# Kernel optimization log

Hardware: AMD Instinct MI355X
Metric: run time of the kernel (lower is better)

The kernel has to match this reference:

```python
import jax, jax.numpy as jnp
import numpy as np

N_NODES = 100000
N_EDGES = 3200000
N_GRAPHS = 64
F_IN = 16
HID = 64


def gcn_conv(x, W, b, src, dst, ew, n_nodes):
    """PyG GCNConv with add_self_loops=True, symmetric normalization.
    x' = D^{-1/2} (A + I) D^{-1/2} (x W) + b, self-loop weight 1."""
    h = x @ W                                             # [N, out]
    deg = jax.ops.segment_sum(ew, dst, num_segments=n_nodes) + 1.0  # self-loop adds 1
    dinv = jax.lax.rsqrt(jnp.maximum(deg, 1e-12))         # deg_inv_sqrt
    norm = dinv[src] * ew * dinv[dst]                     # [E]
    agg = jax.ops.segment_sum(h[src] * norm[:, None], dst, num_segments=n_nodes)
    agg = agg + h * (dinv * dinv)[:, None]                # self-loop term
    return agg + b


def setup_inputs() -> dict:
    key = jax.random.key(0)
    ks = jax.random.split(key, 12)
    x = jax.random.normal(ks[0], (N_NODES, F_IN), dtype=jnp.float32)
    edge_index = jax.random.randint(ks[1], (2, N_EDGES), 0, N_NODES, dtype=jnp.int64)
    edge_weight = jax.random.uniform(ks[2], (N_EDGES,), dtype=jnp.float32)
    batch = jnp.sort(jax.random.randint(ks[3], (N_NODES,), 0, N_GRAPHS, dtype=jnp.int64))
    # GCN layer params (PyG lin: x @ W with W [in, out])
    s1 = 1.0 / np.sqrt(F_IN)
    s2 = 1.0 / np.sqrt(HID)
    W1 = jax.random.uniform(ks[4], (F_IN, HID), jnp.float32, -s1, s1)
    b1 = jnp.zeros((HID,), jnp.float32)
    W2 = jax.random.uniform(ks[5], (HID, HID), jnp.float32, -s2, s2)
    b2 = jnp.zeros((HID,), jnp.float32)
    W3 = jax.random.uniform(ks[6], (HID, HID), jnp.float32, -s2, s2)
    b3 = jnp.zeros((HID,), jnp.float32)
    Wout = jax.random.uniform(ks[7], (HID, 1), jnp.float32, -s2, s2)
    bout = jax.random.uniform(ks[8], (1,), jnp.float32, -s2, s2)
    return {"x": x, "edge_index": edge_index, "edge_weight": edge_weight,
            "batch": batch, "W1": W1, "b1": b1, "W2": W2, "b2": b2,
            "W3": W3, "b3": b3, "Wout": Wout, "bout": bout}


def reference(x, edge_index, edge_weight, batch, W1, b1, W2, b2, W3, b3, Wout, bout):
    src, dst = edge_index[0], edge_index[1]
    n = x.shape[0]
    # layer 1
    h = gcn_conv(x, W1, b1, src, dst, edge_weight, n)
    # layer 2: sigmoid -> (dropout p=0 identity) -> GCNConv
    h = gcn_conv(jax.nn.sigmoid(h), W2, b2, src, dst, edge_weight, n)
    # layer 3
    h = gcn_conv(jax.nn.sigmoid(h), W3, b3, src, dst, edge_weight, n)
    # global mean pool over graphs
    sums = jax.ops.segment_sum(h, batch, num_segments=N_GRAPHS)          # [G, HID]
    counts = jax.ops.segment_sum(jnp.ones((n,), h.dtype), batch, num_segments=N_GRAPHS)
    pooled = sums / jnp.maximum(counts, 1.0)[:, None]
    # final linear head (dropout p=0 identity)
    return pooled @ Wout + bout                                          # [G, 1]
```

## Files before the change

kernel.cpp:

```cpp
#include <hip/hip_runtime.h>
#include <hip/hip_bf16.h>

#define HID 64
#define P_BLOCKS 1024
#define MAXB 512
#define BCAP 9216
#define TILE 3200
#define AGRID 2048

typedef float v2f __attribute__((ext_vector_type(2)));

__device__ inline v2f fp8x2_lo(unsigned u) { return __builtin_amdgcn_cvt_pk_f32_fp8(u, false); }
__device__ inline v2f fp8x2_hi(unsigned u) { return __builtin_amdgcn_cvt_pk_f32_fp8(u, true); }

#define GSCALE 16.0f
#define GINV 0.0625f
#define GS1 12.0f
#define GI1 (1.0f / 12.0f)
#define GS2 24.0f
#define GI2 (1.0f / 24.0f)
#define WQINV (1.0f / 4095.0f)

__global__ __launch_bounds__(256) void kp1a_hist(const int* __restrict__ dst,
                                                 int* __restrict__ ghist,
                                                 int nE, int B, int chunk) {
    __shared__ int h[MAXB];
    for (int b = threadIdx.x; b < B; b += 256) h[b] = 0;
    __syncthreads();
    int lo = blockIdx.x * chunk;
    int hi = min(nE, lo + chunk);
    for (int i = lo + threadIdx.x; i < hi; i += 256)
        atomicAdd(&h[dst[i] >> 8], 1);
    __syncthreads();
    for (int b = threadIdx.x; b < B; b += 256)
        ghist[(size_t)b * P_BLOCKS + blockIdx.x] = h[b];
}

__global__ __launch_bounds__(256) void kp1b1_scan(const int* __restrict__ ghist,
                                                  int* __restrict__ goff,
                                                  int* __restrict__ btot) {
    __shared__ int wsum[4];
    __shared__ int woff[4];
    int tid = threadIdx.x;
    int lane = tid & 63, wv = tid >> 6;
    int b = blockIdx.x;
    int4 v = ((const int4*)(ghist + (size_t)b * P_BLOCKS))[tid];
    int s = v.x + v.y + v.z + v.w;
    int sc = s;
#pragma unroll
    for (int off = 1; off < 64; off <<= 1) {
        int t = __shfl_up(sc, off);
        if (lane >= off) sc += t;
    }
    if (lane == 63) wsum[wv] = sc;
    __syncthreads();
    if (tid == 0) {
        int acc = 0;
#pragma unroll
        for (int w = 0; w < 4; ++w) { woff[w] = acc; acc += wsum[w]; }
        btot[b] = acc;
    }
    __syncthreads();
    int ex = woff[wv] + sc - s;
    int4 o;
    o.x = ex;
    o.y = ex + v.x;
    o.z = o.y + v.y;
    o.w = o.z + v.z;
    ((int4*)(goff + (size_t)b * P_BLOCKS))[tid] = o;
}

__global__ __launch_bounds__(512) void kp1b2_scan(const int* __restrict__ btot,
                                                  int* __restrict__ bstart, int B) {
    __shared__ int wsum[8];
    __shared__ int woff[8];
    int tid = threadIdx.x;
    int lane = tid & 63, wv = tid >> 6;
    int tot = (tid < B) ? btot[tid] : 0;
    int sc = tot;
#pragma unroll
    for (int off = 1; off < 64; off <<= 1) {
        int t = __shfl_up(sc, off);
        if (lane >= off) sc += t;
    }
    if (lane == 63) wsum[wv] = sc;
    __syncthreads();
    if (tid == 0) {
        int acc = 0;
#pragma unroll
        for (int w = 0; w < 8; ++w) { woff[w] = acc; acc += wsum[w]; }
        bstart[B] = acc;
    }
    __syncthreads();
    if (tid < B) bstart[tid] = woff[wv] + sc - tot;
}

__global__ __launch_bounds__(256) void kp1c_sort(const int* __restrict__ src,
                                                 const int* __restrict__ dst,
                                                 const float* __restrict__ ew,
                                                 const int* __restrict__ goff,
                                                 const int* __restrict__ bstart,
                                                 int2* __restrict__ bsw,
                                                 int nE, int B, int chunk) {
    __shared__ int2 sorted[TILE];
    __shared__ unsigned short bkt[TILE];
    __shared__ int cnt[MAXB];
    __shared__ int lstart[MAXB];
    __shared__ int lcur[MAXB];
    __shared__ int gcur[MAXB];
    __shared__ int wsum[4];
    __shared__ int woff[4];
    int tid = threadIdx.x;
    int lane = tid & 63, wv = tid >> 6;
    for (int b = tid; b < B; b += 256)
        gcur[b] = bstart[b] + goff[(size_t)b * P_BLOCKS + blockIdx.x];
    int lo = blockIdx.x * chunk;
    int hi = min(nE, lo + chunk);
    for (int tb = lo; tb < hi; tb += TILE) {
        int m = min(hi - tb, TILE);
        cnt[tid] = 0;
        cnt[tid + 256] = 0;
        __syncthreads();
        for (int i = tid; i < m; i += 256)
            atomicAdd(&cnt[dst[tb + i] >> 8], 1);
        __syncthreads();
        int c0 = cnt[2 * tid], c1 = cnt[2 * tid + 1];
        int s = c0 + c1;
        int sc = s;
#pragma unroll
        for (int off = 1; off < 64; off <<= 1) {
            int t = __shfl_up(sc, off);
            if (lane >= off) sc += t;
        }
        if (lane == 63) wsum[wv] = sc;
        __syncthreads();
        if (tid == 0) {
            int acc = 0;
#pragma unroll
            for (int w = 0; w < 4; ++w) { woff[w] = acc; acc += wsum[w]; }
        }
        __syncthreads();
        int ex = woff[wv] + sc - s;
        lstart[2 * tid] = ex;
        lcur[2 * tid] = ex;
        lstart[2 * tid + 1] = ex + c0;
        lcur[2 * tid + 1] = ex + c0;
        __syncthreads();
        for (int i = tid; i < m; i += 256) {
            int d = dst[tb + i];
            int b = d >> 8;
            int pos = atomicAdd(&lcur[b], 1);
            int2 v;
            v.x = src[tb + i] | ((d & 255) << 20);
            v.y = __float_as_int(ew[tb + i]);
            sorted[pos] = v;
            bkt[pos] = (unsigned short)b;
        }
        __syncthreads();
        for (int i = tid; i < m; i += 256) {
            int b = bkt[i];
            bsw[gcur[b] + (i - lstart[b])] = sorted[i];
        }
        __syncthreads();
        for (int b = tid; b < B; b += 256)
            gcur[b] += lcur[b] - lstart[b];
        __syncthreads();
    }
}

__global__ __launch_bounds__(256) void kp2_build(const int2* __restrict__ bsw,
                                                 const int* __restrict__ bstart,
                                                 int* __restrict__ row_start,
                                                 float* __restrict__ dinv,
                                                 unsigned* __restrict__ csr4,
                                                 int n_nodes) {
    __shared__ int2 ebuf[BCAP];
    __shared__ int cnt[256];
    __shared__ float degw[256];
    __shared__ int cur[256];
    __shared__ int wsum[4];
    __shared__ int woff[4];
    int tid = threadIdx.x;
    int lane = tid & 63, wv = tid >> 6;
    int b = blockIdx.x;
    int e0 = bstart[b], e1 = bstart[b + 1];
    int nb = e1 - e0;
    cnt[tid] = 0;
    degw[tid] = 0.0f;
    __syncthreads();
    for (int i = tid; i < nb; i += 256) {
        int2 v = bsw[e0 + i];
        if (i < BCAP) ebuf[i] = v;
        int dlo = (v.x >> 20) & 255;
        atomicAdd(&cnt[dlo], 1);
        atomicAdd(&degw[dlo], __int_as_float(v.y));
    }
    __syncthreads();
    int c = cnt[tid];
    int sc = c;
#pragma unroll
    for (int off = 1; off < 64; off <<= 1) {
        int t = __shfl_up(sc, off);
        if (lane >= off) sc += t;
    }
    if (lane == 63) wsum[wv] = sc;
    __syncthreads();
    if (tid == 0) {
        int acc = 0;
#pragma unroll
        for (int w = 0; w < 4; ++w) { woff[w] = acc; acc += wsum[w]; }
    }
    __syncthreads();
    int ex = woff[wv] + sc - c;
    cur[tid] = ex;
    int node = (b << 8) + tid;
    if (node < n_nodes) {
        row_start[node] = e0 + ex;
        dinv[node] = rsqrtf(fmaxf(degw[tid] + 1.0f, 1e-12f));
    }
    if (b == 0 && tid == 0) row_start[n_nodes] = bstart[gridDim.x];
    __syncthreads();
    for (int i = tid; i < nb; i += 256) {
        int2 v = (i < BCAP) ? ebuf[i] : bsw[e0 + i];
        int dlo = (v.x >> 20) & 255;
        int pos = atomicAdd(&cur[dlo], 1);
        float w = __int_as_float(v.y);
        unsigned wq = (unsigned)(w * 4095.0f + 0.5f);
        csr4[e0 + pos] = ((unsigned)v.x & 0xFFFFFu) | (wq << 20);
    }
}

__global__ __launch_bounds__(64) void k_wtilde(const float* __restrict__ W3,
                                               const float* __restrict__ Wout,
                                               const float* __restrict__ b3,
                                               float* __restrict__ wtil,
                                               float* __restrict__ c0) {
    int j = threadIdx.x;
    float s = 0.0f;
    for (int k = 0; k < 64; ++k) s += W3[j * 64 + k] * Wout[k];
    wtil[j] = s;
    if (j == 0) {
        float c = 0.0f;
        for (int k = 0; k < 64; ++k) c += b3[k] * Wout[k];
        c0[0] = c;
    }
}

__global__ __launch_bounds__(256) void k_mm16f4(const float* __restrict__ in,
                                                const float* __restrict__ W,
                                                const float* __restrict__ dinv,
                                                unsigned* __restrict__ gtab,
                                                int n_nodes) {
    __shared__ float Ws[16 * HID];
    for (int i = threadIdx.x; i < 16 * HID; i += 256) Ws[i] = W[i];
    __syncthreads();
    int lane = threadIdx.x & 63;
    int wid = threadIdx.x >> 6;
    int p = lane & 7;
    int q = lane >> 3;
    int nGrp = (n_nodes + 7) >> 3;
    for (int grp = blockIdx.x * 4 + wid; grp < nGrp; grp += gridDim.x * 4) {
        int node = grp * 8 + q;
        bool ok = node < n_nodes;
        float xr0 = ok ? in[node * 16 + p] : 0.0f;
        float xr1 = ok ? in[node * 16 + 8 + p] : 0.0f;
        float di = ok ? dinv[node] : 0.0f;
        v2f a01 = {0.0f, 0.0f}, a23 = {0.0f, 0.0f};
        v2f a45 = {0.0f, 0.0f}, a67 = {0.0f, 0.0f};
#pragma unroll
        for (int k = 0; k < 16; ++k) {
            float xv = __shfl((k < 8) ? xr0 : xr1, q * 8 + (k & 7));
            const float4* wr = (const float4*)&Ws[k * HID + 8 * p];
            float4 w0 = wr[0], w1 = wr[1];
            v2f wl0 = {w0.x, w0.y}, wl1 = {w0.z, w0.w};
            v2f wl2 = {w1.x, w1.y}, wl3 = {w1.z, w1.w};
            a01 += wl0 * xv; a23 += wl1 * xv; a45 += wl2 * xv; a67 += wl3 * xv;
        }
        float sc = di * GS1;
        unsigned pk = __builtin_amdgcn_cvt_scalef32_pk_fp4_f32(0u, a01.x * sc, a01.y * sc, 1.0f, 0);
        pk = __builtin_amdgcn_cvt_scalef32_pk_fp4_f32(pk, a23.x * sc, a23.y * sc, 1.0f, 1);
        pk = __builtin_amdgcn_cvt_scalef32_pk_fp4_f32(pk, a45.x * sc, a45.y * sc, 1.0f, 2);
        pk = __builtin_amdgcn_cvt_scalef32_pk_fp4_f32(pk, a67.x * sc, a67.y * sc, 1.0f, 3);
        if (ok) gtab[(size_t)node * 8 + p] = pk;
    }
}

template <int OUT4>
__global__ __launch_bounds__(256) void k_agg4(const unsigned* __restrict__ g4,
                                              const float* __restrict__ bias,
                                              const float* __restrict__ dinv,
                                              const int* __restrict__ row_start,
                                              const unsigned* __restrict__ csr4,
                                              const float* __restrict__ Wn,
                                              void* __restrict__ outv,
                                              int n_nodes, float ginv_in, float gs_out) {
    int lane = threadIdx.x & 63;
    int wid = threadIdx.x >> 6;
    int p = lane & 7;
    int q = lane >> 3;
    int stride = gridDim.x * 4;

    for (int node = blockIdx.x * 4 + wid; node < n_nodes; node += stride) {
        float diRaw = dinv[node];

        v2f a01 = {0.0f, 0.0f}, a23 = {0.0f, 0.0f};
        v2f a45 = {0.0f, 0.0f}, a67 = {0.0f, 0.0f};
        {
            unsigned su = g4[(size_t)node * 8 + p];
            if (q == 0) {
                a01 = __builtin_amdgcn_cvt_scalef32_pk_f32_fp4(su, 1.0f, 0);
                a23 = __builtin_amdgcn_cvt_scalef32_pk_f32_fp4(su, 1.0f, 1);
                a45 = __builtin_amdgcn_cvt_scalef32_pk_f32_fp4(su, 1.0f, 2);
                a67 = __builtin_amdgcn_cvt_scalef32_pk_f32_fp4(su, 1.0f, 3);
            }
        }
        int e0 = row_start[node], e1 = row_start[node + 1];
        for (int base = e0; base < e1; base += 64) {
            int m = min(64, e1 - base);
            unsigned sw = 0;
            if (lane < m) sw = __builtin_nontemporal_load(csr4 + base + lane);
            int ng8 = (m + 7) >> 3;
            int ng84 = (ng8 + 3) & ~3;
            for (int g0 = 0; g0 < ng84; g0 += 4) {
                int b8 = 8 * g0 + q;
                unsigned vA = __shfl(sw, b8);
                unsigned vB = __shfl(sw, b8 + 8);
                unsigned vC = __shfl(sw, b8 + 16);
                unsigned vD = __shfl(sw, b8 + 24);
                unsigned uA = g4[(vA & 0xFFFFFu) * 8u + p];
                unsigned uB = g4[(vB & 0xFFFFFu) * 8u + p];
                unsigned uC = g4[(vC & 0xFFFFFu) * 8u + p];
                unsigned uD = g4[(vD & 0xFFFFFu) * 8u + p];
                float wA = (float)(vA >> 20) * WQINV;
                float wB = (float)(vB >> 20) * WQINV;
                float wC = (float)(vC >> 20) * WQINV;
                float wD = (float)(vD >> 20) * WQINV;
                a01 += __builtin_amdgcn_cvt_scalef32_pk_f32_fp4(uA, 1.0f, 0) * wA;
                a23 += __builtin_amdgcn_cvt_scalef32_pk_f32_fp4(uA, 1.0f, 1) * wA;
                a45 += __builtin_amdgcn_cvt_scalef32_pk_f32_fp4(uA, 1.0f, 2) * wA;
                a67 += __builtin_amdgcn_cvt_scalef32_pk_f32_fp4(uA, 1.0f, 3) * wA;
                a01 += __builtin_amdgcn_cvt_scalef32_pk_f32_fp4(uB, 1.0f, 0) * wB;
                a23 += __builtin_amdgcn_cvt_scalef32_pk_f32_fp4(uB, 1.0f, 1) * wB;
                a45 += __builtin_amdgcn_cvt_scalef32_pk_f32_fp4(uB, 1.0f, 2) * wB;
                a67 += __builtin_amdgcn_cvt_scalef32_pk_f32_fp4(uB, 1.0f, 3) * wB;
                a01 += __builtin_amdgcn_cvt_scalef32_pk_f32_fp4(uC, 1.0f, 0) * wC;
                a23 += __builtin_amdgcn_cvt_scalef32_pk_f32_fp4(uC, 1.0f, 1) * wC;
                a45 += __builtin_amdgcn_cvt_scalef32_pk_f32_fp4(uC, 1.0f, 2) * wC;
                a67 += __builtin_amdgcn_cvt_scalef32_pk_f32_fp4(uC, 1.0f, 3) * wC;
                a01 += __builtin_amdgcn_cvt_scalef32_pk_f32_fp4(uD, 1.0f, 0) * wD;
                a23 += __builtin_amdgcn_cvt_scalef32_pk_f32_fp4(uD, 1.0f, 1) * wD;
                a45 += __builtin_amdgcn_cvt_scalef32_pk_f32_fp4(uD, 1.0f, 2) * wD;
                a67 += __builtin_amdgcn_cvt_scalef32_pk_f32_fp4(uD, 1.0f, 3) * wD;
            }
        }
        float a[8] = {a01.x, a01.y, a23.x, a23.y, a45.x, a45.y, a67.x, a67.y};
#pragma unroll
        for (int i = 0; i < 8; ++i) {
            a[i] += __shfl_xor(a[i], 8);
            a[i] += __shfl_xor(a[i], 16);
            a[i] += __shfl_xor(a[i], 32);
        }
        float di = diRaw * ginv_in;
        float4 bv0 = ((const float4*)bias)[2 * p];
        float4 bv1 = ((const float4*)bias)[2 * p + 1];
        a[0] = fmaf(di, a[0], bv0.x); a[1] = fmaf(di, a[1], bv0.y);
        a[2] = fmaf(di, a[2], bv0.z); a[3] = fmaf(di, a[3], bv0.w);
        a[4] = fmaf(di, a[4], bv1.x); a[5] = fmaf(di, a[5], bv1.y);
        a[6] = fmaf(di, a[6], bv1.z); a[7] = fmaf(di, a[7], bv1.w);
        float s[8];
#pragma unroll
        for (int i = 0; i < 8; ++i) s[i] = 1.0f / (1.0f + __expf(-a[i]));

        if (OUT4) {
            const float4* Wg = (const float4*)Wn;
            v2f o01 = {0.0f, 0.0f}, o23 = {0.0f, 0.0f};
            v2f o45 = {0.0f, 0.0f}, o67 = {0.0f, 0.0f};
#pragma unroll
            for (int st = 0; st < 8; ++st) {
                float av = __shfl(s[st], q);
                const float4* wr = Wg + ((8 * q + st) * 16 + 2 * p);
                float4 w0 = wr[0], w1 = wr[1];
                v2f wl0 = {w0.x, w0.y}, wl1 = {w0.z, w0.w};
                v2f wl2 = {w1.x, w1.y}, wl3 = {w1.z, w1.w};
                o01 += wl0 * av; o23 += wl1 * av; o45 += wl2 * av; o67 += wl3 * av;
            }
            float o[8] = {o01.x, o01.y, o23.x, o23.y, o45.x, o45.y, o67.x, o67.y};
#pragma unroll
            for (int i = 0; i < 8; ++i) {
                o[i] += __shfl_xor(o[i], 8);
                o[i] += __shfl_xor(o[i], 16);
                o[i] += __shfl_xor(o[i], 32);
            }
            if (lane < 8) {
                float sc = diRaw * gs_out;
                unsigned pk = __builtin_amdgcn_cvt_scalef32_pk_fp4_f32(0u, o[0] * sc, o[1] * sc, 1.0f, 0);
                pk = __builtin_amdgcn_cvt_scalef32_pk_fp4_f32(pk, o[2] * sc, o[3] * sc, 1.0f, 1);
                pk = __builtin_amdgcn_cvt_scalef32_pk_fp4_f32(pk, o[4] * sc, o[5] * sc, 1.0f, 2);
                pk = __builtin_amdgcn_cvt_scalef32_pk_fp4_f32(pk, o[6] * sc, o[7] * sc, 1.0f, 3);
                __builtin_nontemporal_store(pk, (unsigned*)outv + (size_t)node * 8 + p);
            }
        } else {
            const float4* wt4 = (const float4*)Wn;
            float4 w0 = wt4[2 * p], w1 = wt4[2 * p + 1];
            float local = s[0] * w0.x + s[1] * w0.y + s[2] * w0.z + s[3] * w0.w
                        + s[4] * w1.x + s[5] * w1.y + s[6] * w1.z + s[7] * w1.w;
            local += __shfl_xor(local, 1);
            local += __shfl_xor(local, 2);
            local += __shfl_xor(local, 4);
            if (lane == 0) {
                unsigned pk = __builtin_amdgcn_cvt_pk_fp8_f32(local * diRaw * gs_out, 0.0f, 0, false);
                ((unsigned char*)outv)[node] = (unsigned char)(pk & 0xFFu);
            }
        }
    }
}

__global__ __launch_bounds__(256) void k_agg3s(const unsigned char* __restrict__ t8,
                                               const int* __restrict__ row_start,
                                               const float* __restrict__ dinv,
                                               const unsigned* __restrict__ csr4,
                                               const float* __restrict__ c0p,
                                               float* __restrict__ p,
                                               int n_nodes) {
    int lane = threadIdx.x & 63;
    int wid = threadIdx.x >> 6;
    int stride = gridDim.x * 4;
    float c0 = c0p[0];
    for (int node = blockIdx.x * 4 + wid; node < n_nodes; node += stride) {
        int e0 = row_start[node], e1 = row_start[node + 1];
        float acc = 0.0f;
        for (int base = e0; base < e1; base += 64) {
            int i = base + lane;
            unsigned sw = (i < e1) ? __builtin_nontemporal_load(csr4 + i) : 0u;
            float tv = fp8x2_lo((unsigned)t8[sw & 0xFFFFFu]).x;
            acc += (float)(sw >> 20) * tv;
        }
        acc *= WQINV;
#pragma unroll
        for (int off = 32; off; off >>= 1) acc += __shfl_xor(acc, off);
        if (lane == 0) {
            float self = fp8x2_lo((unsigned)t8[node]).x;
            p[node] = fmaf(dinv[node] * GINV, acc + self, c0);
        }
    }
}

__global__ __launch_bounds__(256) void k_poolseg(const float* __restrict__ p,
                                                 const int* __restrict__ batch,
                                                 float* __restrict__ psum,
                                                 float* __restrict__ pcnt,
                                                 int n_nodes) {
    int lane = threadIdx.x & 63;
    int gw = (blockIdx.x * blockDim.x + threadIdx.x) >> 6;
    int node = gw * 64 + lane;
    bool valid = node < n_nodes;
    float v = valid ? p[node] : 0.0f;
    int g = valid ? batch[node] : -1;
    int g0 = __shfl(g, 0);
    if (__all((g == g0) && valid)) {
#pragma unroll
        for (int off = 32; off; off >>= 1) v += __shfl_xor(v, off);
        if (lane == 0) {
            atomicAdd(&psum[g0], v);
            atomicAdd(&pcnt[g0], 64.0f);
        }
    } else if (valid) {
        atomicAdd(&psum[g], v);
        atomicAdd(&pcnt[g], 1.0f);
    }
}

__global__ __launch_bounds__(64) void k_out(const float* __restrict__ psum,
                                            const float* __restrict__ pcnt,
                                            const float* __restrict__ bout,
                                            float* __restrict__ out, int G) {
    int g = threadIdx.x;
    if (g < G) out[g] = psum[g] / fmaxf(pcnt[g], 1.0f) + bout[0];
}

extern "C" void kernel_launch(void* const* d_in, const int* in_sizes, int n_in,
                              void* d_out, int out_size, void* d_ws, size_t ws_size,
                              hipStream_t stream) {
    const float* x    = (const float*)d_in[0];
    const int*   eidx = (const int*)d_in[1];
    const float* ew   = (const float*)d_in[2];
    const int*   batch= (const int*)d_in[3];
    const float* W1   = (const float*)d_in[4];
    const float* b1   = (const float*)d_in[5];
    const float* W2   = (const float*)d_in[6];
    const float* b2   = (const float*)d_in[7];
    const float* W3   = (const float*)d_in[8];
    const float* b3   = (const float*)d_in[9];
    const float* Wout = (const float*)d_in[10];
    const float* bout = (const float*)d_in[11];
    float* out = (float*)d_out;

    const int N = in_sizes[0] / 16;
    const int E = in_sizes[2];
    const int G = out_size;
    const int* src = eidx;
    const int* dst = eidx + E;
    const int B = (N + 255) >> 8;
    const int chunk = (E + P_BLOCKS - 1) / P_BLOCKS;

    size_t off = 0;
    auto carve = [&](size_t bytes) -> void* {
        void* p = (char*)d_ws + off;
        off += (bytes + 255) & ~(size_t)255;
        return p;
    };
    float* psum     = (float*)carve(64 * 4);
    float* pcnt     = (float*)carve(64 * 4);
    size_t zero_bytes = off;
    int*   ghist    = (int*)  carve((size_t)B * P_BLOCKS * 4);
    int*   goff     = (int*)  carve((size_t)B * P_BLOCKS * 4);
    int*   btot    = (int*)  carve((size_t)B * 4);
    int*   bstart   = (int*)  carve((size_t)(B + 1) * 4);
    int2*  bsw      = (int2*) carve((size_t)E * 8);
    int*   row_start= (int*)  carve((size_t)(N + 1) * 4);
    unsigned* csr4  = (unsigned*)carve((size_t)E * 4);
    float* dinv     = (float*)carve((size_t)N * 4);
    unsigned* gA    = (unsigned*)carve((size_t)N * HID);
    unsigned* gB    = (unsigned*)carve((size_t)N * HID);
    float* p        = (float*)carve((size_t)N * 4);
    unsigned char* t8 = (unsigned char*)carve((size_t)N + 256);
    float* c0buf    = (float*)carve(256);
    float* wtil     = (float*)carve(64 * 4);
    (void)ws_size;

    (void)hipMemsetAsync(d_ws, 0, zero_bytes, stream);

    const int waveBlocks = ((N + 63) / 64 * 64 + 255) / 256;
    const int mmB4 = (((N + 7) >> 3) + 3) / 4;
    const int aggBlocks = AGRID;

    k_wtilde<<<1, 64, 0, stream>>>(W3, Wout, b3, wtil, c0buf);

    kp1a_hist<<<P_BLOCKS, 256, 0, stream>>>(dst, ghist, E, B, chunk);
    kp1b1_scan<<<B, 256, 0, stream>>>(ghist, goff, btot);
    kp1b2_scan<<<1, 512, 0, stream>>>(btot, bstart, B);
    kp1c_sort<<<P_BLOCKS, 256, 0, stream>>>(src, dst, ew, goff, bstart,
                                            bsw, E, B, chunk);
    kp2_build<<<B, 256, 0, stream>>>(bsw, bstart, row_start, dinv, csr4, N);

    k_mm16f4<<<mmB4, 256, 0, stream>>>(x, W1, dinv, gA, N);
    k_agg4<1><<<aggBlocks, 256, 0, stream>>>(gA, b1, dinv, row_start, csr4,
                                             W2, (void*)gB, N, GI1, GS2);
    k_agg4<0><<<aggBlocks, 256, 0, stream>>>(gB, b2, dinv, row_start, csr4,
                                             wtil, (void*)t8, N, GI2, GSCALE);
    k_agg3s<<<aggBlocks, 256, 0, stream>>>(t8, row_start, dinv, csr4, c0buf,
                                           p, N);

    k_poolseg<<<waveBlocks, 256, 0, stream>>>(p, batch, psum, pcnt, N);
    k_out<<<1, 64, 0, stream>>>(psum, pcnt, bout, out, G);
}
```

Before: 398.0 us.

## Process two nodes per wavefront in aggregation kernels with full-size grid

The aggregation kernels now have each wavefront handle two adjacent nodes together, interleaving their edge loops so twice as many independent gathers are in flight per iteration. The fixed 2048-block grid-stride loop is replaced by a grid sized to cover all nodes once. The epilogue is moved into a shared device helper. This trades higher register pressure, and some wasted lanes when the two nodes have different degrees, for more memory-level parallelism and less loop overhead.

After: 369.1 us. -7.2%, faster.

```diff
diff --git a/kernel.cpp b/kernel.cpp
--- a/kernel.cpp
+++ b/kernel.cpp
@@ -6,7 +6,6 @@
 #define MAXB 512
 #define BCAP 9216
 #define TILE 3200
-#define AGRID 2048
 
 typedef float v2f __attribute__((ext_vector_type(2)));
 
@@ -286,6 +285,81 @@
 }
 
 template <int OUT4>
+__device__ __forceinline__ void agg_epi(int node, int lane, int p, int q,
+                                        float diRaw,
+                                        v2f a01, v2f a23, v2f a45, v2f a67,
+                                        const float* __restrict__ bias,
+                                        const float* __restrict__ Wn,
+                                        void* __restrict__ outv,
+                                        float ginv_in, float gs_out) {
+    float a[8] = {a01.x, a01.y, a23.x, a23.y, a45.x, a45.y, a67.x, a67.y};
+#pragma unroll
+    for (int i = 0; i < 8; ++i) {
+        a[i] += __shfl_xor(a[i], 8);
+        a[i] += __shfl_xor(a[i], 16);
+        a[i] += __shfl_xor(a[i], 32);
+    }
+    float di = diRaw * ginv_in;
+    float4 bv0 = ((const float4*)bias)[2 * p];
+    float4 bv1 = ((const float4*)bias)[2 * p + 1];
+    a[0] = fmaf(di, a[0], bv0.x); a[1] = fmaf(di, a[1], bv0.y);
+    a[2] = fmaf(di, a[2], bv0.z); a[3] = fmaf(di, a[3], bv0.w);
+    a[4] = fmaf(di, a[4], bv1.x); a[5] = fmaf(di, a[5], bv1.y);
+    a[6] = fmaf(di, a[6], bv1.z); a[7] = fmaf(di, a[7], bv1.w);
+    float s[8];
+#pragma unroll
+    for (int i = 0; i < 8; ++i) s[i] = 1.0f / (1.0f + __expf(-a[i]));
+
+    if (OUT4) {
+        const float4* Wg = (const float4*)Wn;
+        v2f o01 = {0.0f, 0.0f}, o23 = {0.0f, 0.0f};
+        v2f o45 = {0.0f, 0.0f}, o67 = {0.0f, 0.0f};
+#pragma unroll
+        for (int st = 0; st < 8; ++st) {
+            float av = __shfl(s[st], q);
+            const float4* wr = Wg + ((8 * q + st) * 16 + 2 * p);
+            float4 w0 = wr[0], w1 = wr[1];
+            v2f wl0 = {w0.x, w0.y}, wl1 = {w0.z, w0.w};
+            v2f wl2 = {w1.x, w1.y}, wl3 = {w1.z, w1.w};
+            o01 += wl0 * av; o23 += wl1 * av; o45 += wl2 * av; o67 += wl3 * av;
+        }
+        float o[8] = {o01.x, o01.y, o23.x, o23.y, o45.x, o45.y, o67.x, o67.y};
+#pragma unroll
+        for (int i = 0; i < 8; ++i) {
+            o[i] += __shfl_xor(o[i], 8);
+            o[i] += __shfl_xor(o[i], 16);
+            o[i] += __shfl_xor(o[i], 32);
+        }
+        if (lane < 8) {
+            float sc = diRaw * gs_out;
+            unsigned pk = __builtin_amdgcn_cvt_scalef32_pk_fp4_f32(0u, o[0] * sc, o[1] * sc, 1.0f, 0);
+            pk = __builtin_amdgcn_cvt_scalef32_pk_fp4_f32(pk, o[2] * sc, o[3] * sc, 1.0f, 1);
+            pk = __builtin_amdgcn_cvt_scalef32_pk_fp4_f32(pk, o[4] * sc, o[5] * sc, 1.0f, 2);
+            pk = __builtin_amdgcn_cvt_scalef32_pk_fp4_f32(pk, o[6] * sc, o[7] * sc, 1.0f, 3);
+            __builtin_nontemporal_store(pk, (unsigned*)outv + (size_t)node * 8 + p);
+        }
+    } else {
+        const float4* wt4 = (const float4*)Wn;
+        float4 w0 = wt4[2 * p], w1 = wt4[2 * p + 1];
+        float local = s[0] * w0.x + s[1] * w0.y + s[2] * w0.z + s[3] * w0.w
+                    + s[4] * w1.x + s[5] * w1.y + s[6] * w1.z + s[7] * w1.w;
+        local += __shfl_xor(local, 1);
+        local += __shfl_xor(local, 2);
+        local += __shfl_xor(local, 4);
+        if (lane == 0) {
+            unsigned pk = __builtin_amdgcn_cvt_pk_fp8_f32(local * diRaw * gs_out, 0.0f, 0, false);
+            ((unsigned char*)outv)[node] = (unsigned char)(pk & 0xFFu);
+        }
+    }
+}
+
+#define ACC_FP4(u, w, a01, a23, a45, a67)                                   \
+    a01 += __builtin_amdgcn_cvt_scalef32_pk_f32_fp4(u, 1.0f, 0) * (w);      \
+    a23 += __builtin_amdgcn_cvt_scalef32_pk_f32_fp4(u, 1.0f, 1) * (w);      \
+    a45 += __builtin_amdgcn_cvt_scalef32_pk_f32_fp4(u, 1.0f, 2) * (w);      \
+    a67 += __builtin_amdgcn_cvt_scalef32_pk_f32_fp4(u, 1.0f, 3) * (w);
+
+template <int OUT4>
 __global__ __launch_bounds__(256) void k_agg4(const unsigned* __restrict__ g4,
                                               const float* __restrict__ bias,
                                               const float* __restrict__ dinv,
@@ -298,121 +372,81 @@
     int wid = threadIdx.x >> 6;
     int p = lane & 7;
     int q = lane >> 3;
-    int stride = gridDim.x * 4;
-
-    for (int node = blockIdx.x * 4 + wid; node < n_nodes; node += stride) {
-        float diRaw = dinv[node];
-
-        v2f a01 = {0.0f, 0.0f}, a23 = {0.0f, 0.0f};
-        v2f a45 = {0.0f, 0.0f}, a67 = {0.0f, 0.0f};
-        {
-            unsigned su = g4[(size_t)node * 8 + p];
-            if (q == 0) {
-                a01 = __builtin_amdgcn_cvt_scalef32_pk_f32_fp4(su, 1.0f, 0);
-                a23 = __builtin_amdgcn_cvt_scalef32_pk_f32_fp4(su, 1.0f, 1);
-                a45 = __builtin_amdgcn_cvt_scalef32_pk_f32_fp4(su, 1.0f, 2);
-                a67 = __builtin_amdgcn_cvt_scalef32_pk_f32_fp4(su, 1.0f, 3);
-            }
-        }
-        int e0 = row_start[node], e1 = row_start[node + 1];
-        for (int base = e0; base < e1; base += 64) {
-            int m = min(64, e1 - base);
-            unsigned sw = 0;
-            if (lane < m) sw = __builtin_nontemporal_load(csr4 + base + lane);
-            int ng8 = (m + 7) >> 3;
-            int ng84 = (ng8 + 3) & ~3;
-            for (int g0 = 0; g0 < ng84; g0 += 4) {
-                int b8 = 8 * g0 + q;
-                unsigned vA = __shfl(sw, b8);
-                unsigned vB = __shfl(sw, b8 + 8);
-                unsigned vC = __shfl(sw, b8 + 16);
-                unsigned vD = __shfl(sw, b8 + 24);
-                unsigned uA = g4[(vA & 0xFFFFFu) * 8u + p];
-                unsigned uB = g4[(vB & 0xFFFFFu) * 8u + p];
-                unsigned uC = g4[(vC & 0xFFFFFu) * 8u + p];
-                unsigned uD = g4[(vD & 0xFFFFFu) * 8u + p];
-                float wA = (float)(vA >> 20) * WQINV;
-                float wB = (float)(vB >> 20) * WQINV;
-                float wC = (float)(vC >> 20) * WQINV;
-                float wD = (float)(vD >> 20) * WQINV;
-                a01 += __builtin_amdgcn_cvt_scalef32_pk_f32_fp4(uA, 1.0f, 0) * wA;
-                a23 += __builtin_amdgcn_cvt_scalef32_pk_f32_fp4(uA, 1.0f, 1) * wA;
-                a45 += __builtin_amdgcn_cvt_scalef32_pk_f32_fp4(uA, 1.0f, 2) * wA;
-                a67 += __builtin_amdgcn_cvt_scalef32_pk_f32_fp4(uA, 1.0f, 3) * wA;
-                a01 += __builtin_amdgcn_cvt_scalef32_pk_f32_fp4(uB, 1.0f, 0) * wB;
-                a23 += __builtin_amdgcn_cvt_scalef32_pk_f32_fp4(uB, 1.0f, 1) * wB;
-                a45 += __builtin_amdgcn_cvt_scalef32_pk_f32_fp4(uB, 1.0f, 2) * wB;
-                a67 += __builtin_amdgcn_cvt_scalef32_pk_f32_fp4(uB, 1.0f, 3) * wB;
-                a01 += __builtin_amdgcn_cvt_scalef32_pk_f32_fp4(uC, 1.0f, 0) * wC;
-                a23 += __builtin_amdgcn_cvt_scalef32_pk_f32_fp4(uC, 1.0f, 1) * wC;
-                a45 += __builtin_amdgcn_cvt_scalef32_pk_f32_fp4(uC, 1.0f, 2) * wC;
-                a67 += __builtin_amdgcn_cvt_scalef32_pk_f32_fp4(uC, 1.0f, 3) * wC;
-                a01 += __builtin_amdgcn_cvt_scalef32_pk_f32_fp4(uD, 1.0f, 0) * wD;
-                a23 += __builtin_amdgcn_cvt_scalef32_pk_f32_fp4(uD, 1.0f, 1) * wD;
-                a45 += __builtin_amdgcn_cvt_scalef32_pk_f32_fp4(uD, 1.0f, 2) * wD;
-                a67 += __builtin_amdgcn_cvt_scalef32_pk_f32_fp4(uD, 1.0f, 3) * wD;
-            }
-        }
-        float a[8] = {a01.x, a01.y, a23.x, a23.y, a45.x, a45.y, a67.x, a67.y};
-#pragma unroll
-        for (int i = 0; i < 8; ++i) {
-            a[i] += __shfl_xor(a[i], 8);
-            a[i] += __shfl_xor(a[i], 16);
-            a[i] += __shfl_xor(a[i], 32);
-        }
-        float di = diRaw * ginv_in;
-        float4 bv0 = ((const float4*)bias)[2 * p];
-        float4 bv1 = ((const float4*)bias)[2 * p + 1];
-        a[0] = fmaf(di, a[0], bv0.x); a[1] = fmaf(di, a[1], bv0.y);
-        a[2] = fmaf(di, a[2], bv0.z); a[3] = fmaf(di, a[3], bv0.w);
-        a[4] = fmaf(di, a[4], bv1.x); a[5] = fmaf(di, a[5], bv1.y);
-        a[6] = fmaf(di, a[6], bv1.z); a[7] = fmaf(di, a[7], bv1.w);
-        float s[8];
-#pragma unroll
-        for (int i = 0; i < 8; ++i) s[i] = 1.0f / (1.0f + __expf(-a[i]));
-
-        if (OUT4) {
-            const float4* Wg = (const float4*)Wn;
-            v2f o01 = {0.0f, 0.0f}, o23 = {0.0f, 0.0f};
-            v2f o45 = {0.0f, 0.0f}, o67 = {0.0f, 0.0f};
-#pragma unroll
-            for (int st = 0; st < 8; ++st) {
-                float av = __shfl(s[st], q);
-                const float4* wr = Wg + ((8 * q + st) * 16 + 2 * p);
-                float4 w0 = wr[0], w1 = wr[1];
-                v2f wl0 = {w0.x, w0.y}, wl1 = {w0.z, w0.w};
-                v2f wl2 = {w1.x, w1.y}, wl3 = {w1.z, w1.w};
-                o01 += wl0 * av; o23 += wl1 * av; o45 += wl2 * av; o67 += wl3 * av;
-            }
-            float o[8] = {o01.x, o01.y, o23.x, o23.y, o45.x, o45.y, o67.x, o67.y};
-#pragma unroll
-            for (int i = 0; i < 8; ++i) {
-                o[i] += __shfl_xor(o[i], 8);
-                o[i] += __shfl_xor(o[i], 16);
-                o[i] += __shfl_xor(o[i], 32);
-            }
-            if (lane < 8) {
-                float sc = diRaw * gs_out;
-                unsigned pk = __builtin_amdgcn_cvt_scalef32_pk_fp4_f32(0u, o[0] * sc, o[1] * sc, 1.0f, 0);
-                pk = __builtin_amdgcn_cvt_scalef32_pk_fp4_f32(pk, o[2] * sc, o[3] * sc, 1.0f, 1);
-                pk = __builtin_amdgcn_cvt_scalef32_pk_fp4_f32(pk, o[4] * sc, o[5] * sc, 1.0f, 2);
-                pk = __builtin_amdgcn_cvt_scalef32_pk_fp4_f32(pk, o[6] * sc, o[7] * sc, 1.0f, 3);
-                __builtin_nontemporal_store(pk, (unsigned*)outv + (size_t)node * 8 + p);
-            }
-        } else {
-            const float4* wt4 = (const float4*)Wn;
-            float4 w0 = wt4[2 * p], w1 = wt4[2 * p + 1];
-            float local = s[0] * w0.x + s[1] * w0.y + s[2] * w0.z + s[3] * w0.w
-                        + s[4] * w1.x + s[5] * w1.y + s[6] * w1.z + s[7] * w1.w;
-            local += __shfl_xor(local, 1);
-            local += __shfl_xor(local, 2);
-            local += __shfl_xor(local, 4);
-            if (lane == 0) {
-                unsigned pk = __builtin_amdgcn_cvt_pk_fp8_f32(local * diRaw * gs_out, 0.0f, 0, false);
-                ((unsigned char*)outv)[node] = (unsigned char)(pk & 0xFFu);
-            }
-        }
-    }
+    int nodeA = (blockIdx.x * 4 + wid) * 2;
+    int nodeB = nodeA + 1;
+    if (nodeA >= n_nodes) return;
+    bool hasB = nodeB < n_nodes;
+
+    float diA = dinv[nodeA];
+    float diB = hasB ? dinv[nodeB] : 0.0f;
+    int rs0 = row_start[nodeA];
+    int rs1 = row_start[nodeA + 1];
+    int rs2 = hasB ? row_start[nodeA + 2] : rs1;
+    unsigned suA = g4[(size_t)nodeA * 8 + p];
+    unsigned suB = hasB ? g4[(size_t)nodeB * 8 + p] : 0u;
+
+    v2f aA01 = {0, 0}, aA23 = {0, 0}, aA45 = {0, 0}, aA67 = {0, 0};
+    v2f aB01 = {0, 0}, aB23 = {0, 0}, aB45 = {0, 0}, aB67 = {0, 0};
+    if (q == 0) {
+        aA01 = __builtin_amdgcn_cvt_scalef32_pk_f32_fp4(suA, 1.0f, 0);
+        aA23 = __builtin_amdgcn_cvt_scalef32_pk_f32_fp4(suA, 1.0f, 1);
+        aA45 = __builtin_amdgcn_cvt_scalef32_pk_f32_fp4(suA, 1.0f, 2);
+        aA67 = __builtin_amdgcn_cvt_scalef32_pk_f32_fp4(suA, 1.0f, 3);
+        aB01 = __builtin_amdgcn_cvt_scalef32_pk_f32_fp4(suB, 1.0f, 0);
+        aB23 = __builtin_amdgcn_cvt_scalef32_pk_f32_fp4(suB, 1.0f, 1);
+        aB45 = __builtin_amdgcn_cvt_scalef32_pk_f32_fp4(suB, 1.0f, 2);
+        aB67 = __builtin_amdgcn_cvt_scalef32_pk_f32_fp4(suB, 1.0f, 3);
+    }
+    int baseA = rs0, e1A = rs1;
+    int baseB = rs1, e1B = rs2;
+    while (baseA < e1A || baseB < e1B) {
+        int mA = (baseA < e1A) ? min(64, e1A - baseA) : 0;
+        int mB = (baseB < e1B) ? min(64, e1B - baseB) : 0;
+        unsigned swA = 0, swB = 0;
+        if (lane < mA) swA = __builtin_nontemporal_load(csr4 + baseA + lane);
+        if (lane < mB) swB = __builtin_nontemporal_load(csr4 + baseB + lane);
+        int ngA = (((mA + 7) >> 3) + 3) & ~3;
+        int ngB = (((mB + 7) >> 3) + 3) & ~3;
+        int ng = max(ngA, ngB);
+        for (int g0 = 0; g0 < ng; g0 += 4) {
+            int b8 = 8 * g0 + q;
+            unsigned vA0 = __shfl(swA, b8),      vB0 = __shfl(swA, b8 + 8);
+            unsigned vC0 = __shfl(swA, b8 + 16), vD0 = __shfl(swA, b8 + 24);
+            unsigned vA1 = __shfl(swB, b8),      vB1 = __shfl(swB, b8 + 8);
+            unsigned vC1 = __shfl(swB, b8 + 16), vD1 = __shfl(swB, b8 + 24);
+            unsigned uA0 = g4[(vA0 & 0xFFFFFu) * 8u + p];
+            unsigned uB0 = g4[(vB0 & 0xFFFFFu) * 8u + p];
+            unsigned uC0 = g4[(vC0 & 0xFFFFFu) * 8u + p];
+            unsigned uD0 = g4[(vD0 & 0xFFFFFu) * 8u + p];
+            unsigned uA1 = g4[(vA1 & 0xFFFFFu) * 8u + p];
+            unsigned uB1 = g4[(vB1 & 0xFFFFFu) * 8u + p];
+            unsigned uC1 = g4[(vC1 & 0xFFFFFu) * 8u + p];
+            unsigned uD1 = g4[(vD1 & 0xFFFFFu) * 8u + p];
+            float wA0 = (float)(vA0 >> 20) * WQINV;
+            float wB0 = (float)(vB0 >> 20) * WQINV;
+            float wC0 = (float)(vC0 >> 20) * WQINV;
+            float wD0 = (float)(vD0 >> 20) * WQINV;
+            float wA1 = (float)(vA1 >> 20) * WQINV;
+            float wB1 = (float)(vB1 >> 20) * WQINV;
+            float wC1 = (float)(vC1 >> 20) * WQINV;
+            float wD1 = (float)(vD1 >> 20) * WQINV;
+            ACC_FP4(uA0, wA0, aA01, aA23, aA45, aA67)
+            ACC_FP4(uB0, wB0, aA01, aA23, aA45, aA67)
+            ACC_FP4(uC0, wC0, aA01, aA23, aA45, aA67)
+            ACC_FP4(uD0, wD0, aA01, aA23, aA45, aA67)
+            ACC_FP4(uA1, wA1, aB01, aB23, aB45, aB67)
+            ACC_FP4(uB1, wB1, aB01, aB23, aB45, aB67)
+            ACC_FP4(uC1, wC1, aB01, aB23, aB45, aB67)
+            ACC_FP4(uD1, wD1, aB01, aB23, aB45, aB67)
+        }
+        baseA += 64;
+        baseB += 64;
+    }
+    agg_epi<OUT4>(nodeA, lane, p, q, diA, aA01, aA23, aA45, aA67,
+                  bias, Wn, outv, ginv_in, gs_out);
+    if (hasB)
+        agg_epi<OUT4>(nodeB, lane, p, q, diB, aB01, aB23, aB45, aB67,
+                      bias, Wn, outv, ginv_in, gs_out);
 }
 
 __global__ __launch_bounds__(256) void k_agg3s(const unsigned char* __restrict__ t8,
@@ -424,23 +458,43 @@
                                                int n_nodes) {
     int lane = threadIdx.x & 63;
     int wid = threadIdx.x >> 6;
-    int stride = gridDim.x * 4;
-    float c0 = c0p[0];
-    for (int node = blockIdx.x * 4 + wid; node < n_nodes; node += stride) {
-        int e0 = row_start[node], e1 = row_start[node + 1];
-        float acc = 0.0f;
-        for (int base = e0; base < e1; base += 64) {
-            int i = base + lane;
-            unsigned sw = (i < e1) ? __builtin_nontemporal_load(csr4 + i) : 0u;
-            float tv = fp8x2_lo((unsigned)t8[sw & 0xFFFFFu]).x;
-            acc += (float)(sw >> 20) * tv;
-        }
-        acc *= WQINV;
-#pragma unroll
-        for (int off = 32; off; off >>= 1) acc += __shfl_xor(acc, off);
-        if (lane == 0) {
-            float self = fp8x2_lo((unsigned)t8[node]).x;
-            p[node] = fmaf(dinv[node] * GINV, acc + self, c0);
+    int nodeA = (blockIdx.x * 4 + wid) * 2;
+    int nodeB = nodeA + 1;
+    if (nodeA >= n_nodes) return;
+    bool hasB = nodeB < n_nodes;
+    int rs0 = row_start[nodeA];
+    int rs1 = row_start[nodeA + 1];
+    int rs2 = hasB ? row_start[nodeA + 2] : rs1;
+    float accA = 0.0f, accB = 0.0f;
+    int baseA = rs0, e1A = rs1;
+    int baseB = rs1, e1B = rs2;
+    while (baseA < e1A || baseB < e1B) {
+        int iA = baseA + lane, iB = baseB + lane;
+        unsigned swA = (baseA < e1A && iA < e1A)
+                           ? __builtin_nontemporal_load(csr4 + iA) : 0u;
+        unsigned swB = (baseB < e1B && iB < e1B)
+                           ? __builtin_nontemporal_load(csr4 + iB) : 0u;
+        float tA = fp8x2_lo((unsigned)t8[swA & 0xFFFFFu]).x;
+        float tB = fp8x2_lo((unsigned)t8[swB & 0xFFFFFu]).x;
+        accA += (float)(swA >> 20) * tA;
+        accB += (float)(swB >> 20) * tB;
+        baseA += 64;
+        baseB += 64;
+    }
+    accA *= WQINV;
+    accB *= WQINV;
+#pragma unroll
+    for (int off = 32; off; off >>= 1) {
+        accA += __shfl_xor(accA, off);
+        accB += __shfl_xor(accB, off);
+    }
+    if (lane == 0) {
+        float c0 = c0p[0];
+        float selfA = fp8x2_lo((unsigned)t8[nodeA]).x;
+        p[nodeA] = fmaf(dinv[nodeA] * GINV, accA + selfA, c0);
+        if (hasB) {
+            float selfB = fp8x2_lo((unsigned)t8[nodeB]).x;
+            p[nodeB] = fmaf(dinv[nodeB] * GINV, accB + selfB, c0);
         }
     }
 }
@@ -530,9 +584,9 @@
 
     (void)hipMemsetAsync(d_ws, 0, zero_bytes, stream);
 
+    const int aggBlocks = ((N + 1) / 2 + 3) / 4;
     const int waveBlocks = ((N + 63) / 64 * 64 + 255) / 256;
     const int mmB4 = (((N + 7) >> 3) + 3) / 4;
-    const int aggBlocks = AGRID;
 
     k_wtilde<<<1, 64, 0, stream>>>(W3, Wout, b3, wtil, c0buf);
 
```
